# Optimization experiments

Measured on AMD Instinct MI355X. Metric: run time of the kernel, lower is better.

## Reference

```python
import jax, jax.numpy as jnp
import numpy as np

B, H, W, C = 64, 56, 56, 256
ROUTES = 4
CONV_OUT = 64


def setup_inputs() -> dict:
    key = jax.random.key(0)
    k1, k2, k3 = jax.random.split(key, 3)
    inputs = jax.random.normal(k1, (B, H, W, C), dtype=jnp.float32)
    # he_normal init for conv kernel (HWIO), zeros bias (keras defaults)
    fan_in = 3 * 3 * C
    conv_w = jax.random.normal(k2, (3, 3, C, CONV_OUT), dtype=jnp.float32) * np.sqrt(2.0 / fan_in)
    conv_b = jnp.zeros((CONV_OUT,), dtype=jnp.float32)
    # glorot_uniform for dense (keras default)
    limit = np.sqrt(6.0 / (CONV_OUT + ROUTES))
    fc_w = jax.random.uniform(k3, (CONV_OUT, ROUTES), dtype=jnp.float32, minval=-limit, maxval=limit)
    fc_b = jnp.zeros((ROUTES,), dtype=jnp.float32)
    return {"inputs": inputs, "conv_w": conv_w, "conv_b": conv_b, "fc_w": fc_w, "fc_b": fc_b}


def reference(inputs, conv_w, conv_b, fc_w, fc_b):
    routes = fc_b.shape[0]
    # route predictor: conv 3x3 stride 2 valid -> global avg pool -> dense logits
    y = jax.lax.conv_general_dilated(
        inputs, conv_w, window_strides=(2, 2), padding="VALID",
        dimension_numbers=("NHWC", "HWIO", "NHWC"))
    y = y + conv_b  # (B, H', W', 64)
    pooled = jnp.mean(y, axis=(1, 2))  # (B, 64)
    logits = pooled @ fc_w + fc_b      # (B, routes)
    route_width = inputs.shape[-1] // routes
    route = jnp.argmax(logits, axis=-1)  # (B,)
    # per-example channel-group gather: channels [r*w, (r+1)*w)
    idx = route[:, None] * route_width + jnp.arange(route_width)  # (B, w)
    x = jnp.take_along_axis(inputs, idx[:, None, None, :], axis=-1)  # (B, H, W, w)
    return (x, logits)
```

## Files before the change

### kernel.cpp

```cpp
#include <hip/hip_runtime.h>
#include <cstdint>
#include <cstddef>

#define Bn 64
#define Hn 56
#define Wn 56
#define Cn 256
#define COn 64
#define RWn 64
#define XSZ ((size_t)Bn * Hn * Wn * RWn)

__global__ __launch_bounds__(256) void kA_bins(
        const float* __restrict__ in, float* __restrict__ spart,
        int NS, int RPS) {
    const int blk   = blockIdx.x;
    const int b     = blk / NS;
    const int split = blk - b * NS;
    const int tid   = threadIdx.x;
    const int lane  = tid & 63;
    const int wave  = tid >> 6;

    const float* base = in + (size_t)b * (Hn * Wn * Cn) + lane * 4;

    float4 acc[9];
#pragma unroll
    for (int k = 0; k < 9; ++k) acc[k] = make_float4(0.f, 0.f, 0.f, 0.f);

    const int h0 = split * RPS;
    for (int h = h0; h < h0 + RPS; ++h) {
        const bool he  = (h & 1) == 0;
        const float rh0 = (he  && h <= 52)            ? 1.f : 0.f;
        const float rh1 = (!he && h <= 53)            ? 1.f : 0.f;
        const float rh2 = (he  && h >= 2 && h <= 54)  ? 1.f : 0.f;
        if (rh0 == 0.f && rh1 == 0.f && rh2 == 0.f) continue;
        const float* rowp = base + (size_t)h * (Wn * Cn);
#pragma unroll
        for (int wb = 0; wb < Wn; wb += 4) {
            const int w = wb + wave;
            const float4 v = *(const float4*)(rowp + (size_t)w * Cn);
            const bool we  = (w & 1) == 0;
            const float cw0 = (we  && w <= 52)           ? 1.f : 0.f;
            const float cw1 = (!we && w <= 53)           ? 1.f : 0.f;
            const float cw2 = (we  && w >= 2 && w <= 54) ? 1.f : 0.f;
            const float wt[9] = { rh0*cw0, rh0*cw1, rh0*cw2,
                                  rh1*cw0, rh1*cw1, rh1*cw2,
                                  rh2*cw0, rh2*cw1, rh2*cw2 };
#pragma unroll
            for (int k = 0; k < 9; ++k) {
                acc[k].x += v.x * wt[k];
                acc[k].y += v.y * wt[k];
                acc[k].z += v.z * wt[k];
                acc[k].w += v.w * wt[k];
            }
        }
    }

    __shared__ float4 lds4[4][9][64];
#pragma unroll
    for (int k = 0; k < 9; ++k) lds4[wave][k][lane] = acc[k];
    __syncthreads();

    const float* ldsf = (const float*)lds4;
    float* op = spart + (((size_t)b * NS + split) * 9) * 256;
#pragma unroll
    for (int k = 0; k < 9; ++k) {
        const float s = ldsf[(0 * 9 + k) * 256 + tid] + ldsf[(1 * 9 + k) * 256 + tid]
                      + ldsf[(2 * 9 + k) * 256 + tid] + ldsf[(3 * 9 + k) * 256 + tid];
        op[k * 256 + tid] = s;
    }
}

__global__ __launch_bounds__(256) void kB_logits(
        const float* __restrict__ spart,
        const float* __restrict__ convw, const float* __restrict__ convb,
        const float* __restrict__ fcw,   const float* __restrict__ fcb,
        float* __restrict__ out_logits, int* __restrict__ routes, int NS) {
    const int b = blockIdx.x;
    const int t = threadIdx.x;
    __shared__ float sS[9 * 256];
    __shared__ float pP[4][64];
    __shared__ float pld[64];
    __shared__ float lgt[4];

    for (int k = 0; k < 9; ++k) {
        float a = 0.f;
        for (int s = 0; s < NS; ++s)
            a += spart[(((size_t)b * NS + s) * 9 + k) * 256 + t];
        sS[k * 256 + t] = a;
    }
    __syncthreads();

    {
        const int co = t & 63, part = t >> 6;
        float a = 0.f;
        for (int k = 0; k < 9; ++k) {
            const int cb = part * 64;
#pragma unroll 8
            for (int ci = 0; ci < 64; ++ci)
                a += sS[k * 256 + cb + ci] * convw[(size_t)(k * 256 + cb + ci) * 64 + co];
        }
        pP[part][co] = a;
    }
    __syncthreads();

    if (t < 64) {
        pld[t] = (pP[0][t] + pP[1][t] + pP[2][t] + pP[3][t]) * (1.f / 729.f) + convb[t];
    }
    __syncthreads();

    if (t < 4) {
        float a = fcb[t];
#pragma unroll
        for (int co = 0; co < 64; ++co) a += pld[co] * fcw[co * 4 + t];
        lgt[t] = a;
        out_logits[b * 4 + t] = a;
    }
    __syncthreads();

    if (t == 0) {
        int bi = 0; float best = lgt[0];
#pragma unroll
        for (int r = 1; r < 4; ++r) if (lgt[r] > best) { best = lgt[r]; bi = r; }
        routes[b] = bi;
    }
}

__global__ __launch_bounds__(256) void kC_gather(
        const float* __restrict__ in, const int* __restrict__ routes,
        float* __restrict__ out) {
    const size_t idx = (size_t)blockIdx.x * 256 + threadIdx.x;
    const size_t pix = idx >> 4;
    const int   f4i  = (int)(idx & 15);
    const int   b    = (int)(pix / (Hn * Wn));
    const int   r    = routes[b];
    const float4 v = *(const float4*)(in + pix * (size_t)Cn + (size_t)r * RWn + (size_t)f4i * 4);
    ((float4*)out)[idx] = v;
}

extern "C" void kernel_launch(void* const* d_in, const int* in_sizes, int n_in,
                              void* d_out, int out_size, void* d_ws, size_t ws_size,
                              hipStream_t stream) {
    const float* in    = (const float*)d_in[0];
    const float* convw = (const float*)d_in[1];
    const float* convb = (const float*)d_in[2];
    const float* fcw   = (const float*)d_in[3];
    const float* fcb   = (const float*)d_in[4];
    float* out = (float*)d_out;

    int NS = 1;
    const int cand[5] = {14, 8, 4, 2, 1};
    for (int i = 0; i < 5; ++i) {
        const size_t need = (size_t)Bn * cand[i] * 9 * 256 * sizeof(float) + 256;
        if (ws_size >= need) { NS = cand[i]; break; }
    }
    const int RPS = Hn / NS;

    float* spart = (float*)d_ws;
    int* routes  = (int*)((char*)d_ws + (size_t)Bn * NS * 9 * 256 * sizeof(float));

    kA_bins  <<<Bn * NS, 256, 0, stream>>>(in, spart, NS, RPS);
    kB_logits<<<Bn,      256, 0, stream>>>(spart, convw, convb, fcw, fcb,
                                           out + XSZ, routes, NS);
    kC_gather<<<12544,   256, 0, stream>>>(in, routes, out);
}
```

Baseline: 376.1 us.

## Replace 9-bin masked accumulation with separable column sums and subtractions

The first kernel now computes per-column sums of even and odd rows, forming the three kernel-row bins by subtracting single boundary rows instead of doing nine masked FMAs per element. The column-bin reduction over width moves into the logits kernel, which applies the same even/odd trick. The grid becomes one block per batch and four columns, and the workspace holds per-column partials instead of per-split partials. This cuts ALU work and makes the kernel bandwidth-bound, at the cost of a few extra boundary-row reads and a larger intermediate buffer read by the second kernel.

```diff
diff --git a/kernel.cpp b/kernel.cpp
--- a/kernel.cpp
+++ b/kernel.cpp
@@ -6,75 +6,54 @@
 #define Hn 56
 #define Wn 56
 #define Cn 256
-#define COn 64
 #define RWn 64
 #define XSZ ((size_t)Bn * Hn * Wn * RWn)
+#define RSTRIDE (Wn * Cn)
 
-__global__ __launch_bounds__(256) void kA_bins(
-        const float* __restrict__ in, float* __restrict__ spart,
-        int NS, int RPS) {
-    const int blk   = blockIdx.x;
-    const int b     = blk / NS;
-    const int split = blk - b * NS;
-    const int tid   = threadIdx.x;
-    const int lane  = tid & 63;
-    const int wave  = tid >> 6;
+__device__ __forceinline__ void f4add(float4& a, const float4& v) {
+    a.x += v.x; a.y += v.y; a.z += v.z; a.w += v.w;
+}
+__device__ __forceinline__ float4 f4sub(const float4& a, const float4& b) {
+    return make_float4(a.x - b.x, a.y - b.y, a.z - b.z, a.w - b.w);
+}
 
-    const float* base = in + (size_t)b * (Hn * Wn * Cn) + lane * 4;
+__global__ __launch_bounds__(256, 4) void kA_col(
+        const float* __restrict__ in, float* __restrict__ V) {
+    const int blk  = blockIdx.x;
+    const int b    = blk / (Wn / 4);
+    const int wg   = blk - b * (Wn / 4);
+    const int lane = threadIdx.x & 63;
+    const int wave = threadIdx.x >> 6;
+    const int w    = wg * 4 + wave;
 
-    float4 acc[9];
+    const float* col = in + ((size_t)b * Hn * Wn + (size_t)w) * Cn + (size_t)lane * 4;
+
+    float4 A = make_float4(0.f, 0.f, 0.f, 0.f);
+    float4 B = make_float4(0.f, 0.f, 0.f, 0.f);
 #pragma unroll
-    for (int k = 0; k < 9; ++k) acc[k] = make_float4(0.f, 0.f, 0.f, 0.f);
+    for (int h = 0; h < Hn; h += 2) {
+        f4add(A, *(const float4*)(col + (size_t)h * RSTRIDE));
+        f4add(B, *(const float4*)(col + (size_t)(h + 1) * RSTRIDE));
+    }
+    const float4 r0  = *(const float4*)(col);
+    const float4 r54 = *(const float4*)(col + (size_t)54 * RSTRIDE);
+    const float4 r55 = *(const float4*)(col + (size_t)55 * RSTRIDE);
 
-    const int h0 = split * RPS;
-    for (int h = h0; h < h0 + RPS; ++h) {
-        const bool he  = (h & 1) == 0;
-        const float rh0 = (he  && h <= 52)            ? 1.f : 0.f;
-        const float rh1 = (!he && h <= 53)            ? 1.f : 0.f;
-        const float rh2 = (he  && h >= 2 && h <= 54)  ? 1.f : 0.f;
-        if (rh0 == 0.f && rh1 == 0.f && rh2 == 0.f) continue;
-        const float* rowp = base + (size_t)h * (Wn * Cn);
-#pragma unroll
-        for (int wb = 0; wb < Wn; wb += 4) {
-            const int w = wb + wave;
-            const float4 v = *(const float4*)(rowp + (size_t)w * Cn);
-            const bool we  = (w & 1) == 0;
-            const float cw0 = (we  && w <= 52)           ? 1.f : 0.f;
-            const float cw1 = (!we && w <= 53)           ? 1.f : 0.f;
-            const float cw2 = (we  && w >= 2 && w <= 54) ? 1.f : 0.f;
-            const float wt[9] = { rh0*cw0, rh0*cw1, rh0*cw2,
-                                  rh1*cw0, rh1*cw1, rh1*cw2,
-                                  rh2*cw0, rh2*cw1, rh2*cw2 };
-#pragma unroll
-            for (int k = 0; k < 9; ++k) {
-                acc[k].x += v.x * wt[k];
-                acc[k].y += v.y * wt[k];
-                acc[k].z += v.z * wt[k];
-                acc[k].w += v.w * wt[k];
-            }
-        }
-    }
+    const float4 T0 = f4sub(A, r54);
+    const float4 T2 = f4sub(A, r0);
+    const float4 T1 = f4sub(B, r55);
 
-    __shared__ float4 lds4[4][9][64];
-#pragma unroll
-    for (int k = 0; k < 9; ++k) lds4[wave][k][lane] = acc[k];
-    __syncthreads();
-
-    const float* ldsf = (const float*)lds4;
-    float* op = spart + (((size_t)b * NS + split) * 9) * 256;
-#pragma unroll
-    for (int k = 0; k < 9; ++k) {
-        const float s = ldsf[(0 * 9 + k) * 256 + tid] + ldsf[(1 * 9 + k) * 256 + tid]
-                      + ldsf[(2 * 9 + k) * 256 + tid] + ldsf[(3 * 9 + k) * 256 + tid];
-        op[k * 256 + tid] = s;
-    }
+    float4* op = (float4*)(V + (((size_t)b * Wn + w) * 3) * 256) + lane;
+    op[0]       = T0;
+    op[64]      = T1;
+    op[128]     = T2;
 }
 
 __global__ __launch_bounds__(256) void kB_logits(
-        const float* __restrict__ spart,
+        const float* __restrict__ V,
         const float* __restrict__ convw, const float* __restrict__ convb,
         const float* __restrict__ fcw,   const float* __restrict__ fcb,
-        float* __restrict__ out_logits, int* __restrict__ routes, int NS) {
+        float* __restrict__ out_logits, int* __restrict__ routes) {
     const int b = blockIdx.x;
     const int t = threadIdx.x;
     __shared__ float sS[9 * 256];
@@ -82,17 +61,32 @@
     __shared__ float pld[64];
     __shared__ float lgt[4];
 
-    for (int k = 0; k < 9; ++k) {
-        float a = 0.f;
-        for (int s = 0; s < NS; ++s)
-            a += spart[(((size_t)b * NS + s) * 9 + k) * 256 + t];
-        sS[k * 256 + t] = a;
+    const float* Vb = V + (size_t)b * Wn * 3 * 256;
+    float Ae[3] = {0.f, 0.f, 0.f};
+    float Bo[3] = {0.f, 0.f, 0.f};
+#pragma unroll
+    for (int w = 0; w < Wn; w += 2) {
+#pragma unroll
+        for (int kh = 0; kh < 3; ++kh) {
+            Ae[kh] += Vb[((w    ) * 3 + kh) * 256 + t];
+            Bo[kh] += Vb[((w + 1) * 3 + kh) * 256 + t];
+        }
+    }
+#pragma unroll
+    for (int kh = 0; kh < 3; ++kh) {
+        const float t0  = Vb[(0  * 3 + kh) * 256 + t];
+        const float t54 = Vb[(54 * 3 + kh) * 256 + t];
+        const float t55 = Vb[(55 * 3 + kh) * 256 + t];
+        sS[(kh * 3 + 0) * 256 + t] = Ae[kh] - t54;
+        sS[(kh * 3 + 1) * 256 + t] = Bo[kh] - t55;
+        sS[(kh * 3 + 2) * 256 + t] = Ae[kh] - t0;
     }
     __syncthreads();
 
     {
         const int co = t & 63, part = t >> 6;
         float a = 0.f;
+#pragma unroll
         for (int k = 0; k < 9; ++k) {
             const int cb = part * 64;
 #pragma unroll 8
@@ -103,9 +97,8 @@
     }
     __syncthreads();
 
-    if (t < 64) {
+    if (t < 64)
         pld[t] = (pP[0][t] + pP[1][t] + pP[2][t] + pP[3][t]) * (1.f / 729.f) + convb[t];
-    }
     __syncthreads();
 
     if (t < 4) {
@@ -133,7 +126,8 @@
     const int   f4i  = (int)(idx & 15);
     const int   b    = (int)(pix / (Hn * Wn));
     const int   r    = routes[b];
-    const float4 v = *(const float4*)(in + pix * (size_t)Cn + (size_t)r * RWn + (size_t)f4i * 4);
+    const float4 v = *(const float4*)(in + pix * (size_t)Cn
+                                      + (size_t)r * RWn + (size_t)f4i * 4);
     ((float4*)out)[idx] = v;
 }
 
@@ -147,19 +141,12 @@
     const float* fcb   = (const float*)d_in[4];
     float* out = (float*)d_out;
 
-    int NS = 1;
-    const int cand[5] = {14, 8, 4, 2, 1};
-    for (int i = 0; i < 5; ++i) {
-        const size_t need = (size_t)Bn * cand[i] * 9 * 256 * sizeof(float) + 256;
-        if (ws_size >= need) { NS = cand[i]; break; }
-    }
-    const int RPS = Hn / NS;
+    const size_t vBytes = (size_t)Bn * Wn * 3 * 256 * sizeof(float);
+    float* V      = (float*)d_ws;
+    int*   routes = (int*)((char*)d_ws + vBytes);
 
-    float* spart = (float*)d_ws;
-    int* routes  = (int*)((char*)d_ws + (size_t)Bn * NS * 9 * 256 * sizeof(float));
-
-    kA_bins  <<<Bn * NS, 256, 0, stream>>>(in, spart, NS, RPS);
-    kB_logits<<<Bn,      256, 0, stream>>>(spart, convw, convb, fcw, fcb,
-                                           out + XSZ, routes, NS);
-    kC_gather<<<12544,   256, 0, stream>>>(in, routes, out);
+    kA_col   <<<Bn * (Wn / 4), 256, 0, stream>>>(in, V);
+    kB_logits<<<Bn,            256, 0, stream>>>(V, convw, convb, fcw, fcb,
+                                                 out + XSZ, routes);
+    kC_gather<<<12544,         256, 0, stream>>>(in, routes, out);
 }
```

After: 350.6 us. 1.07x faster.
